# Kernel tuning notes

Measured on AMD Instinct MI355X. Metric: run time of the kernel, lower is better.

The kernel has to match this reference:

```python
import jax, jax.numpy as jnp
import numpy as np

N_NODES = 100000
N_EDGES = 1600000
D = 128
R = 3
L = 3


def setup_inputs() -> dict:
    key = jax.random.key(0)
    ks = jax.random.split(key, 6)
    features = jax.random.normal(ks[0], (N_NODES, D), dtype=jnp.float32)
    # per-layer relation weights [L, R, D, D], self-loop weights [L, D, D], bias [L, D]
    W = jax.random.normal(ks[1], (L, R, D, D), dtype=jnp.float32) * 0.05
    W_self = jax.random.normal(ks[2], (L, D, D), dtype=jnp.float32) * 0.05
    bias = jnp.zeros((L, D), dtype=jnp.float32)
    src = jax.random.randint(ks[3], (N_EDGES,), 0, N_NODES, dtype=jnp.int32)
    dst = jax.random.randint(ks[4], (N_EDGES,), 0, N_NODES, dtype=jnp.int32)
    etypes = jax.random.randint(ks[5], (N_EDGES,), 0, R, dtype=jnp.int32)
    return {"features": features, "W": W, "W_self": W_self, "bias": bias,
            "src": src, "dst": dst, "etypes": etypes}


def _rel_graph_conv(h, Wl, Wsl, bl, src, dst, etypes):
    # Transform all nodes under every relation once: [N, R, D]
    xW = jnp.einsum('ni,rio->nro', h, Wl)
    # Per-edge message = transformed source feature under edge's relation: [E, D]
    msg = xW[src, etypes]
    # Scatter-add aggregation onto destination nodes
    agg = jax.ops.segment_sum(msg, dst, num_segments=N_NODES)
    # Self-loop + bias (DGL RelGraphConv defaults: self_loop=True, bias=True)
    return agg + h @ Wsl + bl


def reference(features, W, W_self, bias, src, dst, etypes):
    h = features
    for l in range(L):
        h = _rel_graph_conv(h, W[l], W_self[l], bias[l], src, dst, etypes)
    return h
```

## Files before the change

### kernel.cpp

```cpp
#include <hip/hip_runtime.h>


#define DD 128

typedef __attribute__((ext_vector_type(8))) short short8;
typedef __attribute__((ext_vector_type(4))) float f32x4;
typedef __attribute__((ext_vector_type(4))) unsigned int u32x4;

__device__ __forceinline__ float bf2f(ushort u) {
    return __uint_as_float(((unsigned)u) << 16);
}
__device__ __forceinline__ ushort f2bf(float f) {
    unsigned b = __float_as_uint(f);
    return (ushort)((b + 0x7FFFu + ((b >> 16) & 1u)) >> 16);
}
__device__ __forceinline__ unsigned packbf(float f) {
    ushort hi = f2bf(f);
    ushort lo = f2bf(f - bf2f(hi));
    return (unsigned)hi | ((unsigned)lo << 16);
}
__device__ __forceinline__ float hi_f(unsigned u) { return __uint_as_float(u << 16); }
__device__ __forceinline__ float lo_f(unsigned u) { return __uint_as_float(u & 0xffff0000u); }
__device__ __forceinline__ float both_f(unsigned u) { return hi_f(u) + lo_f(u); }

#define GLOAD_LDS16(g, l)                                                      \
    __builtin_amdgcn_global_load_lds(                                          \
        (const __attribute__((address_space(1))) void*)(g),                    \
        (__attribute__((address_space(3))) void*)(l), 16, 0, 0)

__global__ __launch_bounds__(256) void k_split_feat(
    const float* __restrict__ feat, unsigned* __restrict__ h_il, int n4)
{
    int i = blockIdx.x * 256 + threadIdx.x;
    if (i >= n4) return;
    float4 v = reinterpret_cast<const float4*>(feat)[i];
    u32x4 p;
    p.x = packbf(v.x); p.y = packbf(v.y); p.z = packbf(v.z); p.w = packbf(v.w);
    reinterpret_cast<u32x4*>(h_il)[i] = p;
}

__global__ __launch_bounds__(256) void k_build_bimg(
    const float* __restrict__ W, const float* __restrict__ Wself,
    ushort* __restrict__ bh, ushort* __restrict__ bl_)
{
    int idx = blockIdx.x * 256 + threadIdx.x;
    if (idx >= 3 * 65536) return;
    int l = idx >> 16, rem = idx & 65535;
    int j = rem & 7, v = (rem >> 3) & 63, g = (rem >> 9) & 7, c = (rem >> 12) & 15;
    int col = g * 16 + (v & 15);
    int k = c * 32 + ((v >> 4) * 8) + j;
    float val;
    if (k < 128) val = Wself[((size_t)l * 128 + k) * 128 + col];
    else {
        int kk = k - 128, r = kk >> 7, i = kk & 127;
        val = W[(((size_t)l * 3 + r) * 128 + i) * 128 + col];
    }
    ushort hi = f2bf(val);
    ushort lo = f2bf(val - bf2f(hi));
    bh[idx] = hi; bl_[idx] = lo;
}

__global__ __launch_bounds__(256) void k_zero(int* __restrict__ p, int n) {
    int i = blockIdx.x * 256 + threadIdx.x;
    if (i < n) p[i] = 0;
}
__global__ __launch_bounds__(256) void k_hist3(
    const int* __restrict__ dst, const int* __restrict__ et,
    int* __restrict__ deg, int nEdges) {
    int e = blockIdx.x * 256 + threadIdx.x;
    if (e < nEdges) atomicAdd(&deg[dst[e] * 3 + et[e]], 1);
}
__global__ __launch_bounds__(1024) void k_scanA(
    const int* __restrict__ deg, int* __restrict__ off,
    int* __restrict__ chunkSum, int n) {
    __shared__ int s[1024];
    const int tid = threadIdx.x;
    const int i = blockIdx.x * 1024 + tid;
    int v = (i < n) ? deg[i] : 0;
    s[tid] = v;
    __syncthreads();
    for (int o = 1; o < 1024; o <<= 1) {
        int t = (tid >= o) ? s[tid - o] : 0;
        __syncthreads();
        s[tid] += t;
        __syncthreads();
    }
    if (i < n) off[i] = s[tid] - v;
    if (tid == 1023) chunkSum[blockIdx.x] = s[1023];
}
__global__ __launch_bounds__(512) void k_scanB(int* __restrict__ chunkSum, int nChunks) {
    __shared__ int s[512];
    const int tid = threadIdx.x;
    int v = (tid < nChunks) ? chunkSum[tid] : 0;
    s[tid] = v;
    __syncthreads();
    for (int o = 1; o < 512; o <<= 1) {
        int t = (tid >= o) ? s[tid - o] : 0;
        __syncthreads();
        s[tid] += t;
        __syncthreads();
    }
    if (tid < nChunks) chunkSum[tid] = s[tid] - v;
}
__global__ __launch_bounds__(256) void k_scanC(
    int* __restrict__ off, int* __restrict__ pos,
    const int* __restrict__ chunkBase, int n, int total) {
    int i = blockIdx.x * 256 + threadIdx.x;
    if (i < n) {
        int o = off[i] + chunkBase[i >> 10];
        off[i] = o;
        pos[i] = o;
    }
    if (i == 0) off[n] = total;
}
__global__ __launch_bounds__(256) void k_scatter3(
    const int* __restrict__ src, const int* __restrict__ dst,
    const int* __restrict__ et, int* __restrict__ pos,
    int* __restrict__ csr, int nEdges) {
    int e = blockIdx.x * 256 + threadIdx.x;
    if (e < nEdges) {
        int j = atomicAdd(&pos[dst[e] * 3 + et[e]], 1);
        csr[j] = src[e];
    }
}

__global__ __launch_bounds__(256) void rgcn_gather(
    const unsigned* __restrict__ h_il,
    const int* __restrict__ off3, const int* __restrict__ csr,
    unsigned* __restrict__ aggF_il,
    int nNodes)
{
    const int gtid = blockIdx.x * 256 + threadIdx.x;
    const int gw   = gtid >> 6;
    const int lane = threadIdx.x & 63;
    const int sub  = lane >> 5;
    const int li   = lane & 31;
    const int n    = gw * 2 + sub;
    if (n >= nNodes) return;
    const int e0 = li * 4;

    #pragma unroll
    for (int r = 0; r < 3; ++r) {
        const int b = off3[n * 3 + r];
        const int e = off3[n * 3 + r + 1];
        float ax = 0.f, ay = 0.f, az = 0.f, aw = 0.f;
        int j = b;
        for (; j + 3 < e; j += 4) {
            int s0 = csr[j], s1 = csr[j + 1], s2 = csr[j + 2], s3 = csr[j + 3];
            u32x4 v0 = *reinterpret_cast<const u32x4*>(h_il + (size_t)s0 * DD + e0);
            u32x4 v1 = *reinterpret_cast<const u32x4*>(h_il + (size_t)s1 * DD + e0);
            u32x4 v2 = *reinterpret_cast<const u32x4*>(h_il + (size_t)s2 * DD + e0);
            u32x4 v3 = *reinterpret_cast<const u32x4*>(h_il + (size_t)s3 * DD + e0);
            ax += (both_f(v0.x) + both_f(v1.x)) + (both_f(v2.x) + both_f(v3.x));
            ay += (both_f(v0.y) + both_f(v1.y)) + (both_f(v2.y) + both_f(v3.y));
            az += (both_f(v0.z) + both_f(v1.z)) + (both_f(v2.z) + both_f(v3.z));
            aw += (both_f(v0.w) + both_f(v1.w)) + (both_f(v2.w) + both_f(v3.w));
        }
        for (; j < e; ++j) {
            int s0 = csr[j];
            u32x4 v0 = *reinterpret_cast<const u32x4*>(h_il + (size_t)s0 * DD + e0);
            ax += both_f(v0.x); ay += both_f(v0.y);
            az += both_f(v0.z); aw += both_f(v0.w);
        }
        u32x4 p;
        p.x = packbf(ax); p.y = packbf(ay); p.z = packbf(az); p.w = packbf(aw);
        __builtin_nontemporal_store(
            p, reinterpret_cast<u32x4*>(aggF_il + (size_t)n * 384 + r * DD + e0));
    }
}

__global__ __launch_bounds__(256) void rgcn_mfma(
    const unsigned* __restrict__ h_il,
    const unsigned* __restrict__ aggF_il,
    const ushort* __restrict__ bimg_hi, const ushort* __restrict__ bimg_lo,
    const float* __restrict__ bl,
    unsigned* __restrict__ out_il,
    float* __restrict__ out_f32,
    int isFinal, int nNodes)
{
    __shared__ unsigned As[2][4096];

    const int t = threadIdx.x;
    const int w = t >> 6;
    const int lane = t & 63;
    const int wr = w >> 1, wc = w & 1;
    const int row0 = blockIdx.x * 128;

    f32x4 acc[4][4];
    #pragma unroll
    for (int i = 0; i < 4; ++i)
        #pragma unroll
        for (int jn = 0; jn < 4; ++jn) acc[i][jn] = f32x4{0.f, 0.f, 0.f, 0.f};

    const int arow0 = row0 + (2 * w) * 16 + (lane & 15);
    const int arow1 = row0 + (2 * w + 1) * 16 + (lane & 15);
    const int ak    = (lane >> 4) * 8;

#define STAGE_A(CH, BUF)                                                           \
    {                                                                              \
        const int kc_ = (CH) * 32;                                                 \
        const unsigned* sP_; int strideU_; int kloc_;                              \
        if (kc_ < 128) { sP_ = h_il; strideU_ = DD; kloc_ = kc_; }                 \
        else { sP_ = aggF_il; strideU_ = 384; kloc_ = kc_ - 128; }                 \
        const unsigned* s0_ = sP_ + (size_t)arow0 * strideU_ + kloc_ + ak;         \
        const unsigned* s1_ = sP_ + (size_t)arow1 * strideU_ + kloc_ + ak;         \
        GLOAD_LDS16(s0_,     &As[BUF][(2 * w) * 512]);                             \
        GLOAD_LDS16(s0_ + 4, &As[BUF][(2 * w) * 512 + 256]);                       \
        GLOAD_LDS16(s1_,     &As[BUF][(2 * w + 1) * 512]);                         \
        GLOAD_LDS16(s1_ + 4, &As[BUF][(2 * w + 1) * 512 + 256]);                   \
    }

    STAGE_A(0, 0);
    __syncthreads();

    for (int ch = 0; ch < 16; ++ch) {
        const int cur = ch & 1;
        if (ch < 15) STAGE_A(ch + 1, cur ^ 1);

        short8 bh[4], blo[4];
        #pragma unroll
        for (int jn = 0; jn < 4; ++jn) {
            const size_t base = ((size_t)(ch * 8 + wc * 4 + jn) * 64 + lane) * 8;
            bh[jn]  = *reinterpret_cast<const short8*>(bimg_hi + base);
            blo[jn] = *reinterpret_cast<const short8*>(bimg_lo + base);
        }
        short8 ah[4], al[4];
        #pragma unroll
        for (int i = 0; i < 4; ++i) {
            const unsigned* tb = &As[cur][(wr * 4 + i) * 512];
            u32x4 q0 = *reinterpret_cast<const u32x4*>(tb + lane * 4);
            u32x4 q1 = *reinterpret_cast<const u32x4*>(tb + 256 + lane * 4);
            u32x4 AH, AL;
            AH.x = (q0.x & 0xffffu) | (q0.y << 16);
            AH.y = (q0.z & 0xffffu) | (q0.w << 16);
            AH.z = (q1.x & 0xffffu) | (q1.y << 16);
            AH.w = (q1.z & 0xffffu) | (q1.w << 16);
            AL.x = (q0.x >> 16) | (q0.y & 0xffff0000u);
            AL.y = (q0.z >> 16) | (q0.w & 0xffff0000u);
            AL.z = (q1.x >> 16) | (q1.y & 0xffff0000u);
            AL.w = (q1.z >> 16) | (q1.w & 0xffff0000u);
            ah[i] = __builtin_bit_cast(short8, AH);
            al[i] = __builtin_bit_cast(short8, AL);
        }
        #pragma unroll
        for (int i = 0; i < 4; ++i)
            #pragma unroll
            for (int jn = 0; jn < 4; ++jn) {
                acc[i][jn] = __builtin_amdgcn_mfma_f32_16x16x32_bf16(ah[i], bh[jn],  acc[i][jn], 0, 0, 0);
                acc[i][jn] = __builtin_amdgcn_mfma_f32_16x16x32_bf16(ah[i], blo[jn], acc[i][jn], 0, 0, 0);
                acc[i][jn] = __builtin_amdgcn_mfma_f32_16x16x32_bf16(al[i], bh[jn],  acc[i][jn], 0, 0, 0);
            }
        __syncthreads();
    }
#undef STAGE_A

    const int colb = wc * 64 + (lane & 15);
    const int rowb = row0 + wr * 64 + (lane >> 4) * 4;
    #pragma unroll
    for (int i = 0; i < 4; ++i) {
        #pragma unroll
        for (int jn = 0; jn < 4; ++jn) {
            const int col = colb + jn * 16;
            const float bb = bl[col];
            #pragma unroll
            for (int rr = 0; rr < 4; ++rr) {
                const int row = rowb + i * 16 + rr;
                if (row < nNodes) {
                    const float v = acc[i][jn][rr] + bb;
                    if (isFinal) {
                        __builtin_nontemporal_store(v, out_f32 + (size_t)row * DD + col);
                    } else {
                        out_il[(size_t)row * DD + col] = packbf(v);
                    }
                }
            }
        }
    }
}

extern "C" void kernel_launch(void* const* d_in, const int* in_sizes, int n_in,
                              void* d_out, int out_size, void* d_ws, size_t ws_size,
                              hipStream_t stream) {
    const float* feat  = (const float*)d_in[0];
    const float* W     = (const float*)d_in[1];
    const float* Wself = (const float*)d_in[2];
    const float* bias  = (const float*)d_in[3];
    const int*   src   = (const int*)d_in[4];
    const int*   dst   = (const int*)d_in[5];
    const int*   et    = (const int*)d_in[6];
    float* out = (float*)d_out;

    const int nNodes = in_sizes[0] / DD;
    const int nEdges = in_sizes[4];
    const int nBins  = nNodes * 3;

    unsigned* h_il    = (unsigned*)d_ws;
    unsigned* aggF_il = h_il + (size_t)nNodes * DD;
    ushort* bimg_hi   = (ushort*)(aggF_il + (size_t)nNodes * 384);
    ushort* bimg_lo   = bimg_hi + 3 * 65536;
    int* ip = (int*)(bimg_lo + 3 * 65536);
    int* deg3     = ip;
    int* off3     = deg3 + nBins;
    int* pos3     = off3 + nBins + 1;
    int* chunkSum = pos3 + nBins;
    int* csr      = chunkSum + 512;

    const int nChunks = (nBins + 1023) / 1024;
    const int nEB = (nEdges + 255) / 256;
    const int nBB = (nBins + 255) / 256;

    const int n4 = nNodes * DD / 4;
    k_split_feat<<<(n4 + 255) / 256, 256, 0, stream>>>(feat, h_il, n4);
    k_build_bimg<<<(3 * 65536 + 255) / 256, 256, 0, stream>>>(W, Wself, bimg_hi, bimg_lo);

    k_zero    <<<nBB, 256, 0, stream>>>(deg3, nBins);
    k_hist3   <<<nEB, 256, 0, stream>>>(dst, et, deg3, nEdges);
    k_scanA   <<<nChunks, 1024, 0, stream>>>(deg3, off3, chunkSum, nBins);
    k_scanB   <<<1, 512, 0, stream>>>(chunkSum, nChunks);
    k_scanC   <<<nBB, 256, 0, stream>>>(off3, pos3, chunkSum, nBins, nEdges);
    k_scatter3<<<nEB, 256, 0, stream>>>(src, dst, et, pos3, csr, nEdges);

    const int gatherBlocks = (nNodes + 7) / 8;
    const int gemmBlocks   = (nNodes + 127) / 128;

    for (int l = 0; l < 3; ++l) {
        rgcn_gather<<<gatherBlocks, 256, 0, stream>>>(
            h_il, off3, csr, aggF_il, nNodes);
        rgcn_mfma<<<gemmBlocks, 256, 0, stream>>>(
            h_il, aggF_il,
            bimg_hi + l * 65536, bimg_lo + l * 65536,
            bias + (size_t)l * DD,
            h_il, out, (l == 2) ? 1 : 0, nNodes);
    }
}
```

Baseline: 904.0 us.

## Load A fragments directly from global memory instead of LDS double-buffering

The MFMA GEMM kernel no longer stages the A operand (hi/lo bf16 split features and aggregates) through a double-buffered LDS tile with global_load_lds and per-chunk barriers. Each wave now reads its A fragments straight from global memory into registers, the 16-chunk K loop is fully unrolled, and launch bounds request two blocks per SIMD. This drops barrier and LDS traffic, but the two waves sharing a row block now both fetch the same A rows from global or L2. Full unrolling plus the register cap could also raise register pressure or cause spills.

```diff
diff --git a/kernel.cpp b/kernel.cpp
--- a/kernel.cpp
+++ b/kernel.cpp
@@ -22,11 +22,6 @@
 __device__ __forceinline__ float hi_f(unsigned u) { return __uint_as_float(u << 16); }
 __device__ __forceinline__ float lo_f(unsigned u) { return __uint_as_float(u & 0xffff0000u); }
 __device__ __forceinline__ float both_f(unsigned u) { return hi_f(u) + lo_f(u); }
-
-#define GLOAD_LDS16(g, l)                                                      \
-    __builtin_amdgcn_global_load_lds(                                          \
-        (const __attribute__((address_space(1))) void*)(g),                    \
-        (__attribute__((address_space(3))) void*)(l), 16, 0, 0)
 
 __global__ __launch_bounds__(256) void k_split_feat(
     const float* __restrict__ feat, unsigned* __restrict__ h_il, int n4)
@@ -169,7 +164,7 @@
     }
 }
 
-__global__ __launch_bounds__(256) void rgcn_mfma(
+__global__ __launch_bounds__(256, 2) void rgcn_mfma(
     const unsigned* __restrict__ h_il,
     const unsigned* __restrict__ aggF_il,
     const ushort* __restrict__ bimg_hi, const ushort* __restrict__ bimg_lo,
@@ -178,8 +173,6 @@
     float* __restrict__ out_f32,
     int isFinal, int nNodes)
 {
-    __shared__ unsigned As[2][4096];
-
     const int t = threadIdx.x;
     const int w = t >> 6;
     const int lane = t & 63;
@@ -192,44 +185,26 @@
         #pragma unroll
         for (int jn = 0; jn < 4; ++jn) acc[i][jn] = f32x4{0.f, 0.f, 0.f, 0.f};
 
-    const int arow0 = row0 + (2 * w) * 16 + (lane & 15);
-    const int arow1 = row0 + (2 * w + 1) * 16 + (lane & 15);
-    const int ak    = (lane >> 4) * 8;
-
-#define STAGE_A(CH, BUF)                                                           \
-    {                                                                              \
-        const int kc_ = (CH) * 32;                                                 \
-        const unsigned* sP_; int strideU_; int kloc_;                              \
-        if (kc_ < 128) { sP_ = h_il; strideU_ = DD; kloc_ = kc_; }                 \
-        else { sP_ = aggF_il; strideU_ = 384; kloc_ = kc_ - 128; }                 \
-        const unsigned* s0_ = sP_ + (size_t)arow0 * strideU_ + kloc_ + ak;         \
-        const unsigned* s1_ = sP_ + (size_t)arow1 * strideU_ + kloc_ + ak;         \
-        GLOAD_LDS16(s0_,     &As[BUF][(2 * w) * 512]);                             \
-        GLOAD_LDS16(s0_ + 4, &As[BUF][(2 * w) * 512 + 256]);                       \
-        GLOAD_LDS16(s1_,     &As[BUF][(2 * w + 1) * 512]);                         \
-        GLOAD_LDS16(s1_ + 4, &As[BUF][(2 * w + 1) * 512 + 256]);                   \
-    }
-
-    STAGE_A(0, 0);
-    __syncthreads();
-
+    const int rloc = lane & 15;
+    const int ak   = (lane >> 4) * 8;
+    const unsigned* rowH[4];
+    const unsigned* rowA[4];
+    #pragma unroll
+    for (int i = 0; i < 4; ++i) {
+        const int gr = row0 + (wr * 4 + i) * 16 + rloc;
+        rowH[i] = h_il    + (size_t)gr * DD  + ak;
+        rowA[i] = aggF_il + (size_t)gr * 384 + ak;
+    }
+
+    #pragma unroll
     for (int ch = 0; ch < 16; ++ch) {
-        const int cur = ch & 1;
-        if (ch < 15) STAGE_A(ch + 1, cur ^ 1);
-
-        short8 bh[4], blo[4];
-        #pragma unroll
-        for (int jn = 0; jn < 4; ++jn) {
-            const size_t base = ((size_t)(ch * 8 + wc * 4 + jn) * 64 + lane) * 8;
-            bh[jn]  = *reinterpret_cast<const short8*>(bimg_hi + base);
-            blo[jn] = *reinterpret_cast<const short8*>(bimg_lo + base);
-        }
         short8 ah[4], al[4];
         #pragma unroll
         for (int i = 0; i < 4; ++i) {
-            const unsigned* tb = &As[cur][(wr * 4 + i) * 512];
-            u32x4 q0 = *reinterpret_cast<const u32x4*>(tb + lane * 4);
-            u32x4 q1 = *reinterpret_cast<const u32x4*>(tb + 256 + lane * 4);
+            const unsigned* p = (ch < 4) ? (rowH[i] + ch * 32)
+                                         : (rowA[i] + (ch - 4) * 32);
+            u32x4 q0 = *reinterpret_cast<const u32x4*>(p);
+            u32x4 q1 = *reinterpret_cast<const u32x4*>(p + 4);
             u32x4 AH, AL;
             AH.x = (q0.x & 0xffffu) | (q0.y << 16);
             AH.y = (q0.z & 0xffffu) | (q0.w << 16);
@@ -242,6 +217,13 @@
             ah[i] = __builtin_bit_cast(short8, AH);
             al[i] = __builtin_bit_cast(short8, AL);
         }
+        short8 bh[4], blo[4];
+        #pragma unroll
+        for (int jn = 0; jn < 4; ++jn) {
+            const size_t base = ((size_t)(ch * 8 + wc * 4 + jn) * 64 + lane) * 8;
+            bh[jn]  = *reinterpret_cast<const short8*>(bimg_hi + base);
+            blo[jn] = *reinterpret_cast<const short8*>(bimg_lo + base);
+        }
         #pragma unroll
         for (int i = 0; i < 4; ++i)
             #pragma unroll
@@ -250,9 +232,7 @@
                 acc[i][jn] = __builtin_amdgcn_mfma_f32_16x16x32_bf16(ah[i], blo[jn], acc[i][jn], 0, 0, 0);
                 acc[i][jn] = __builtin_amdgcn_mfma_f32_16x16x32_bf16(al[i], bh[jn],  acc[i][jn], 0, 0, 0);
             }
-        __syncthreads();
-    }
-#undef STAGE_A
+    }
 
     const int colb = wc * 64 + (lane & 15);
     const int rowb = row0 + wr * 64 + (lane >> 4) * 4;
```

New measurement: 0.9996 ms. +10.6%, slower.
